# Optimization experiments

Measured on AMD Instinct MI355X. Metric: run time of the kernel, lower is better.

Reference implementation:

```python
import jax, jax.numpy as jnp
import numpy as np

TEMPERATURE = 0.07
SIM_THRESHOLD = 0.5


def setup_inputs() -> dict:
    key = jax.random.key(0)
    k1, k2 = jax.random.split(key)
    features = jax.random.normal(k1, (4096, 2, 128), dtype=jnp.float32)
    labels = jax.random.randint(k2, (4096, 100), 0, 2).astype(jnp.float32)
    return {"features": features, "labels": labels}


def reference(features, labels):
    B, V, D = features.shape

    # label Jaccard similarity -> positive/negative masks [B, B]
    intersection = labels @ labels.T
    row_sum = jnp.sum(labels, axis=1, keepdims=True)
    union = row_sum + row_sum.T - intersection
    similarity = intersection / (union + 1e-6)
    positive_mask = (similarity >= SIM_THRESHOLD).astype(jnp.float32)
    negative_mask = 1.0 - positive_mask

    # torch.cat(torch.unbind(features, dim=1), dim=0) -> [V*B, D] (view-major)
    contrast_feature = jnp.transpose(features, (1, 0, 2)).reshape(V * B, D)
    dot_similarities = (contrast_feature @ contrast_feature.T) / TEMPERATURE  # [VB, VB]

    # numerical stability: subtract detached row max over the FULL row
    logits_max = jax.lax.stop_gradient(jnp.max(dot_similarities, axis=1, keepdims=True))
    logits = dot_similarities - logits_max

    # only the top-left [B, B] block is ever indexed by the original loop
    e = jnp.exp(logits[:B, :B])
    pos_sum = jnp.sum(e * positive_mask, axis=1)  # [B]
    neg_sum = jnp.sum(e * negative_mask, axis=1)  # [B]

    has_pos = jnp.sum(positive_mask, axis=1) > 0  # rows with >=1 positive
    pos_safe = jnp.where(has_pos, pos_sum, 1.0)
    den_safe = jnp.where(has_pos, pos_sum + neg_sum, 1.0)
    per_row = -jnp.log(pos_safe / den_safe)

    count = jnp.sum(has_pos.astype(jnp.float32))
    loss = jnp.sum(jnp.where(has_pos, per_row, 0.0)) / jnp.maximum(count, 1.0)
    return loss
```

## Files before the change

### kernel.cpp

```cpp
#include <hip/hip_runtime.h>
#include <math.h>

#define B_ROWS 4096
#define DIM 128
#define LBL 100
#define NCHUNK 16
#define NTILE 32

typedef __attribute__((ext_vector_type(8))) short bf16x8;
typedef __attribute__((ext_vector_type(4))) float f32x4;

__device__ __forceinline__ unsigned f2bf(float x) {
  union { float f; unsigned u; } a; a.f = x;
  unsigned r = a.u + 0x7fffu + ((a.u >> 16) & 1u);
  return r >> 16;
}

__device__ __forceinline__ void lds_dma16(void* l, const void* g) {
  __builtin_amdgcn_global_load_lds(
      (const __attribute__((address_space(1))) void*)g,
      (__attribute__((address_space(3))) void*)l, 16, 0, 0);
}

__global__ void pack_kernel(const float* __restrict__ feat,
                            uint4* __restrict__ cf) {
  int g = blockIdx.x * 256 + threadIdx.x;
  int tile = g >> 11, o = g & 2047;
  int kc = o >> 7, q = o & 127;
  int r = q ^ kc;
  const float* src = feat + ((size_t)(tile * 128 + r)) * 256 + kc * 8;
  float4 a = *(const float4*)src;
  float4 b = *(const float4*)(src + 4);
  uint4 ov;
  ov.x = f2bf(a.x) | (f2bf(a.y) << 16);
  ov.y = f2bf(a.z) | (f2bf(a.w) << 16);
  ov.z = f2bf(b.x) | (f2bf(b.y) << 16);
  ov.w = f2bf(b.z) | (f2bf(b.w) << 16);
  cf[g] = ov;
}

__global__ void seedlabel_kernel(const float* __restrict__ feat,
                                 const float* __restrict__ labels,
                                 uint4* __restrict__ Lb,
                                 int* __restrict__ rsv,
                                 float* __restrict__ seedRaw) {
  int w = (int)((blockIdx.x * blockDim.x + threadIdx.x) >> 6);
  int lane = threadIdx.x & 63;
  const float2* src = (const float2*)(feat + (size_t)w * 256);
  float2 f = src[lane];
  float b0 = __uint_as_float(f2bf(f.x) << 16);
  float b1 = __uint_as_float(f2bf(f.y) << 16);
  float s = b0 * b0 + b1 * b1;
  #pragma unroll
  for (int off = 32; off >= 1; off >>= 1) s += __shfl_xor(s, off);
  float x0 = labels[(size_t)w * LBL + lane];
  float x1 = (lane < LBL - 64) ? labels[(size_t)w * LBL + 64 + lane] : 0.0f;
  unsigned long long m0 = __ballot(x0 != 0.0f);
  unsigned long long m1 = __ballot(x1 != 0.0f);
  if (lane == 0) {
    Lb[w] = make_uint4((unsigned)m0, (unsigned)(m0 >> 32),
                       (unsigned)m1, (unsigned)(m1 >> 32));
    rsv[w] = __popcll(m0) + __popcll(m1);
    seedRaw[w] = s - 0.15f;
  }
}

__launch_bounds__(256, 2)
__global__ void main_kernel(const uint4* __restrict__ cf,
                            const uint4* __restrict__ Lb,
                            const int* __restrict__ rsv,
                            const float* __restrict__ seedRaw,
                            float2* __restrict__ part) {
  __shared__ uint4 As[2048];
  __shared__ uint4 Bs[2048];
  const int tid = threadIdx.x;
  const int lane = tid & 63;
  const int l15 = lane & 15;
  const int quad = lane >> 4;
  const int wave = tid >> 6;
  const int wi = (wave & 1) * 64;
  const int wj = (wave >> 1) * 64;
  const int rowBase = blockIdx.x * 128;
  const float invT = 1.0f / 0.07f;

  #pragma unroll
  for (int it = 0; it < 8; ++it) {
    int flat = it * 256 + tid;
    lds_dma16(&As[flat], &cf[(size_t)blockIdx.x * 2048 + flat]);
  }

  float srow[16], p_s[16], n_s[16];
  #pragma unroll
  for (int ti = 0; ti < 4; ++ti)
    #pragma unroll
    for (int r = 0; r < 4; ++r) {
      srow[ti * 4 + r] = seedRaw[rowBase + wi + ti * 16 + quad * 4 + r];
      p_s[ti * 4 + r] = 0.f;
      n_s[ti * 4 + r] = 0.f;
    }

  const bf16x8* Asv = (const bf16x8*)As;
  const bf16x8* Bsv = (const bf16x8*)Bs;

  for (int jt = 0; jt < 2; ++jt) {
    const int colBase = blockIdx.y * 256 + jt * 128;
    __syncthreads();
    #pragma unroll
    for (int it = 0; it < 8; ++it) {
      int flat = it * 256 + tid;
      lds_dma16(&Bs[flat], &cf[(size_t)(colBase >> 7) * 2048 + flat]);
    }
    __syncthreads();

    uint4 clb[4];
    int crs[4];
    #pragma unroll
    for (int tj = 0; tj < 4; ++tj) {
      int gcol = colBase + wj + tj * 16 + l15;
      clb[tj] = Lb[gcol];
      crs[tj] = rsv[gcol];
    }

    f32x4 acc[4][4];
    #pragma unroll
    for (int ti = 0; ti < 4; ++ti)
      #pragma unroll
      for (int tj = 0; tj < 4; ++tj)
        acc[ti][tj] = (f32x4){0.f, 0.f, 0.f, 0.f};

    #pragma unroll
    for (int ks = 0; ks < 4; ++ks) {
      const int kc = ks * 4 + quad;
      const int abase = kc * 128 + wi + (l15 ^ kc);
      const int bbase = kc * 128 + wj + (l15 ^ kc);
      bf16x8 af[4], bfr[4];
      #pragma unroll
      for (int t = 0; t < 4; ++t) {
        af[t] = Asv[abase + t * 16];
        bfr[t] = Bsv[bbase + t * 16];
      }
      #pragma unroll
      for (int ti = 0; ti < 4; ++ti)
        #pragma unroll
        for (int tj = 0; tj < 4; ++tj)
          acc[ti][tj] = __builtin_amdgcn_mfma_f32_16x16x32_bf16(
              af[ti], bfr[tj], acc[ti][tj], 0, 0, 0);
    }

    #pragma unroll
    for (int ti = 0; ti < 4; ++ti)
      #pragma unroll
      for (int r = 0; r < 4; ++r) {
        int si = ti * 4 + r;
        float l0 = acc[ti][0][r], l1 = acc[ti][1][r];
        float l2 = acc[ti][2][r], l3 = acc[ti][3][r];
        float tm = fmaxf(fmaxf(l0, l1), fmaxf(l2, l3));
        if (tm > srow[si] - 6.3f) {
          int grow = rowBase + wi + ti * 16 + quad * 4 + r;
          uint4 la = Lb[grow];
          int ra = rsv[grow];
          float p = p_s[si], n = n_s[si];
          float lv[4] = {l0, l1, l2, l3};
          #pragma unroll
          for (int tj = 0; tj < 4; ++tj) {
            float e = __expf((lv[tj] - srow[si]) * invT);
            int inter = __popc(la.x & clb[tj].x) + __popc(la.y & clb[tj].y) +
                        __popc(la.z & clb[tj].z) + __popc(la.w & clb[tj].w);
            if (3 * inter > ra + crs[tj]) p += e; else n += e;
          }
          p_s[si] = p;
          n_s[si] = n;
        }
      }
  }

  #pragma unroll
  for (int si = 0; si < 16; ++si) {
    float p = p_s[si], n = n_s[si];
    #pragma unroll
    for (int off = 8; off >= 1; off >>= 1) {
      p += __shfl_xor(p, off);
      n += __shfl_xor(n, off);
    }
    p_s[si] = p;
    n_s[si] = n;
  }

  __syncthreads();
  float* mbuf = (float*)As;
  if (wj == 64 && l15 == 0) {
    #pragma unroll
    for (int ti = 0; ti < 4; ++ti)
      #pragma unroll
      for (int r = 0; r < 4; ++r) {
        int row = wi + ti * 16 + quad * 4 + r;
        int si = ti * 4 + r;
        mbuf[row * 2 + 0] = p_s[si];
        mbuf[row * 2 + 1] = n_s[si];
      }
  }
  __syncthreads();
  if (wj == 0 && l15 == 0) {
    #pragma unroll
    for (int ti = 0; ti < 4; ++ti)
      #pragma unroll
      for (int r = 0; r < 4; ++r) {
        int row = wi + ti * 16 + quad * 4 + r;
        int si = ti * 4 + r;
        float p = p_s[si] + mbuf[row * 2 + 0];
        float n = n_s[si] + mbuf[row * 2 + 1];
        part[(size_t)blockIdx.y * B_ROWS + rowBase + row] = make_float2(p, n);
      }
  }
}

__global__ void mergefin_kernel(const float2* __restrict__ part,
                                const int* __restrict__ rsv,
                                float* __restrict__ out) {
  __shared__ float red[8];
  int t = threadIdx.x;
  float per = 0.f, cnt = 0.f;
  #pragma unroll
  for (int i = 0; i < 16; ++i) {
    int row = i * 256 + t;
    float p = 0.f, n = 0.f;
    #pragma unroll
    for (int c = 0; c < NCHUNK; ++c) {
      float2 v = part[(size_t)c * B_ROWS + row];
      p += v.x;
      n += v.y;
    }
    if (rsv[row] > 0) {
      per += -logf(p / (p + n));
      cnt += 1.f;
    }
  }
  #pragma unroll
  for (int off = 32; off >= 1; off >>= 1) {
    per += __shfl_xor(per, off);
    cnt += __shfl_xor(cnt, off);
  }
  int wv = t >> 6;
  if ((t & 63) == 0) { red[wv * 2] = per; red[wv * 2 + 1] = cnt; }
  __syncthreads();
  if (t == 0) {
    float P = red[0] + red[2] + red[4] + red[6];
    float C = red[1] + red[3] + red[5] + red[7];
    out[0] = P / fmaxf(C, 1.0f);
  }
}

extern "C" void kernel_launch(void* const* d_in, const int* in_sizes, int n_in,
                              void* d_out, int out_size, void* d_ws, size_t ws_size,
                              hipStream_t stream) {
  const float* feat = (const float*)d_in[0];
  const float* labels = (const float*)d_in[1];
  float* out = (float*)d_out;
  char* ws = (char*)d_ws;
  uint4* cf = (uint4*)(ws + 0);
  uint4* Lbm = (uint4*)(ws + 1048576);
  int* rsv = (int*)(ws + 1114112);
  float* seedRaw = (float*)(ws + 1130496);
  float2* part = (float2*)(ws + 1146880);

  hipLaunchKernelGGL(pack_kernel, dim3(256), dim3(256), 0, stream, feat, cf);
  hipLaunchKernelGGL(seedlabel_kernel, dim3(1024), dim3(256), 0, stream,
                     feat, labels, Lbm, rsv, seedRaw);
  hipLaunchKernelGGL(main_kernel, dim3(NTILE, NCHUNK), dim3(256), 0, stream,
                     cf, Lbm, rsv, seedRaw, part);
  hipLaunchKernelGGL(mergefin_kernel, dim3(1), dim3(256), 0, stream,
                     part, rsv, out);
}
```

Before: 86.25 us.

## Use 32x32 one-tile-per-block grid, stage labels in LDS, parallelize merge with atomics

The main kernel now processes a single 128x128 tile per block on a 32x32 grid instead of two column tiles per block on a 32x16 grid. Both A and B tiles are loaded up front, and row and column label bitmasks, popcounts and seeds are staged once in shared memory. The pack kernel remaps thread indexing so global reads are coalesced per row and writes go to the swizzled layout. The single-block merge is replaced by a 16-block merge using atomics plus a tiny finish kernel. This adds more parallelism and removes serial tail work, at the cost of twice as many partial sums and an extra kernel launch.

Measured after the change: 85.01 us. About the same (-1.4%).

```diff
diff --git a/kernel.cpp b/kernel.cpp
--- a/kernel.cpp
+++ b/kernel.cpp
@@ -4,8 +4,7 @@
 #define B_ROWS 4096
 #define DIM 128
 #define LBL 100
-#define NCHUNK 16
-#define NTILE 32
+#define NCT 32
 
 typedef __attribute__((ext_vector_type(8))) short bf16x8;
 typedef __attribute__((ext_vector_type(4))) float f32x4;
@@ -23,11 +22,12 @@
 }
 
 __global__ void pack_kernel(const float* __restrict__ feat,
-                            uint4* __restrict__ cf) {
+                            uint4* __restrict__ cf,
+                            float* __restrict__ accum) {
+  if (blockIdx.x == 0 && threadIdx.x < 2) accum[threadIdx.x] = 0.0f;
   int g = blockIdx.x * 256 + threadIdx.x;
-  int tile = g >> 11, o = g & 2047;
-  int kc = o >> 7, q = o & 127;
-  int r = q ^ kc;
+  int tile = g >> 11, rem = g & 2047;
+  int r = rem >> 4, kc = rem & 15;
   const float* src = feat + ((size_t)(tile * 128 + r)) * 256 + kc * 8;
   float4 a = *(const float4*)src;
   float4 b = *(const float4*)(src + 4);
@@ -36,7 +36,7 @@
   ov.y = f2bf(a.z) | (f2bf(a.w) << 16);
   ov.z = f2bf(b.x) | (f2bf(b.y) << 16);
   ov.w = f2bf(b.z) | (f2bf(b.w) << 16);
-  cf[g] = ov;
+  cf[(size_t)tile * 2048 + kc * 128 + (r ^ kc)] = ov;
 }
 
 __global__ void seedlabel_kernel(const float* __restrict__ feat,
@@ -73,6 +73,11 @@
                             float2* __restrict__ part) {
   __shared__ uint4 As[2048];
   __shared__ uint4 Bs[2048];
+  __shared__ uint4 cLb[128];
+  __shared__ uint4 rLb[128];
+  __shared__ int   cRs[128];
+  __shared__ int   rRs[128];
+  __shared__ float sS[128];
   const int tid = threadIdx.x;
   const int lane = tid & 63;
   const int l15 = lane & 15;
@@ -81,98 +86,92 @@
   const int wi = (wave & 1) * 64;
   const int wj = (wave >> 1) * 64;
   const int rowBase = blockIdx.x * 128;
+  const int colBase = blockIdx.y * 128;
   const float invT = 1.0f / 0.07f;
 
   #pragma unroll
   for (int it = 0; it < 8; ++it) {
     int flat = it * 256 + tid;
     lds_dma16(&As[flat], &cf[(size_t)blockIdx.x * 2048 + flat]);
-  }
-
-  float srow[16], p_s[16], n_s[16];
+    lds_dma16(&Bs[flat], &cf[(size_t)blockIdx.y * 2048 + flat]);
+  }
+  if (tid < 128) {
+    cLb[tid] = Lb[colBase + tid];
+    cRs[tid] = rsv[colBase + tid];
+    sS[tid] = seedRaw[rowBase + tid];
+  } else {
+    int t = tid - 128;
+    rLb[t] = Lb[rowBase + t];
+    rRs[t] = rsv[rowBase + t];
+  }
+  __syncthreads();
+
+  float srow[16];
   #pragma unroll
   for (int ti = 0; ti < 4; ++ti)
     #pragma unroll
-    for (int r = 0; r < 4; ++r) {
-      srow[ti * 4 + r] = seedRaw[rowBase + wi + ti * 16 + quad * 4 + r];
-      p_s[ti * 4 + r] = 0.f;
-      n_s[ti * 4 + r] = 0.f;
-    }
+    for (int r = 0; r < 4; ++r)
+      srow[ti * 4 + r] = sS[wi + ti * 16 + quad * 4 + r];
 
   const bf16x8* Asv = (const bf16x8*)As;
   const bf16x8* Bsv = (const bf16x8*)Bs;
 
-  for (int jt = 0; jt < 2; ++jt) {
-    const int colBase = blockIdx.y * 256 + jt * 128;
-    __syncthreads();
-    #pragma unroll
-    for (int it = 0; it < 8; ++it) {
-      int flat = it * 256 + tid;
-      lds_dma16(&Bs[flat], &cf[(size_t)(colBase >> 7) * 2048 + flat]);
+  f32x4 acc[4][4];
+  #pragma unroll
+  for (int ti = 0; ti < 4; ++ti)
+    #pragma unroll
+    for (int tj = 0; tj < 4; ++tj)
+      acc[ti][tj] = (f32x4){0.f, 0.f, 0.f, 0.f};
+
+  #pragma unroll
+  for (int ks = 0; ks < 4; ++ks) {
+    const int kc = ks * 4 + quad;
+    const int abase = kc * 128 + wi + (l15 ^ kc);
+    const int bbase = kc * 128 + wj + (l15 ^ kc);
+    bf16x8 af[4], bfr[4];
+    #pragma unroll
+    for (int t = 0; t < 4; ++t) {
+      af[t] = Asv[abase + t * 16];
+      bfr[t] = Bsv[bbase + t * 16];
     }
-    __syncthreads();
-
-    uint4 clb[4];
-    int crs[4];
-    #pragma unroll
-    for (int tj = 0; tj < 4; ++tj) {
-      int gcol = colBase + wj + tj * 16 + l15;
-      clb[tj] = Lb[gcol];
-      crs[tj] = rsv[gcol];
-    }
-
-    f32x4 acc[4][4];
     #pragma unroll
     for (int ti = 0; ti < 4; ++ti)
       #pragma unroll
       for (int tj = 0; tj < 4; ++tj)
-        acc[ti][tj] = (f32x4){0.f, 0.f, 0.f, 0.f};
-
-    #pragma unroll
-    for (int ks = 0; ks < 4; ++ks) {
-      const int kc = ks * 4 + quad;
-      const int abase = kc * 128 + wi + (l15 ^ kc);
-      const int bbase = kc * 128 + wj + (l15 ^ kc);
-      bf16x8 af[4], bfr[4];
-      #pragma unroll
-      for (int t = 0; t < 4; ++t) {
-        af[t] = Asv[abase + t * 16];
-        bfr[t] = Bsv[bbase + t * 16];
+        acc[ti][tj] = __builtin_amdgcn_mfma_f32_16x16x32_bf16(
+            af[ti], bfr[tj], acc[ti][tj], 0, 0, 0);
+  }
+
+  float p_s[16], n_s[16];
+  #pragma unroll
+  for (int i = 0; i < 16; ++i) { p_s[i] = 0.f; n_s[i] = 0.f; }
+  #pragma unroll
+  for (int ti = 0; ti < 4; ++ti)
+    #pragma unroll
+    for (int r = 0; r < 4; ++r) {
+      int si = ti * 4 + r;
+      float l0 = acc[ti][0][r], l1 = acc[ti][1][r];
+      float l2 = acc[ti][2][r], l3 = acc[ti][3][r];
+      float tm = fmaxf(fmaxf(l0, l1), fmaxf(l2, l3));
+      if (tm > srow[si] - 6.3f) {
+        int lrow = wi + ti * 16 + quad * 4 + r;
+        uint4 la = rLb[lrow];
+        int ra = rRs[lrow];
+        float p = 0.f, n = 0.f;
+        float lv[4] = {l0, l1, l2, l3};
+        #pragma unroll
+        for (int tj = 0; tj < 4; ++tj) {
+          float e = __expf((lv[tj] - srow[si]) * invT);
+          int lcol = wj + tj * 16 + l15;
+          uint4 lb = cLb[lcol];
+          int inter = __popc(la.x & lb.x) + __popc(la.y & lb.y) +
+                      __popc(la.z & lb.z) + __popc(la.w & lb.w);
+          if (3 * inter > ra + cRs[lcol]) p += e; else n += e;
+        }
+        p_s[si] = p;
+        n_s[si] = n;
       }
-      #pragma unroll
-      for (int ti = 0; ti < 4; ++ti)
-        #pragma unroll
-        for (int tj = 0; tj < 4; ++tj)
-          acc[ti][tj] = __builtin_amdgcn_mfma_f32_16x16x32_bf16(
-              af[ti], bfr[tj], acc[ti][tj], 0, 0, 0);
     }
-
-    #pragma unroll
-    for (int ti = 0; ti < 4; ++ti)
-      #pragma unroll
-      for (int r = 0; r < 4; ++r) {
-        int si = ti * 4 + r;
-        float l0 = acc[ti][0][r], l1 = acc[ti][1][r];
-        float l2 = acc[ti][2][r], l3 = acc[ti][3][r];
-        float tm = fmaxf(fmaxf(l0, l1), fmaxf(l2, l3));
-        if (tm > srow[si] - 6.3f) {
-          int grow = rowBase + wi + ti * 16 + quad * 4 + r;
-          uint4 la = Lb[grow];
-          int ra = rsv[grow];
-          float p = p_s[si], n = n_s[si];
-          float lv[4] = {l0, l1, l2, l3};
-          #pragma unroll
-          for (int tj = 0; tj < 4; ++tj) {
-            float e = __expf((lv[tj] - srow[si]) * invT);
-            int inter = __popc(la.x & clb[tj].x) + __popc(la.y & clb[tj].y) +
-                        __popc(la.z & clb[tj].z) + __popc(la.w & clb[tj].w);
-            if (3 * inter > ra + crs[tj]) p += e; else n += e;
-          }
-          p_s[si] = p;
-          n_s[si] = n;
-        }
-      }
-  }
 
   #pragma unroll
   for (int si = 0; si < 16; ++si) {
@@ -214,40 +213,36 @@
   }
 }
 
-__global__ void mergefin_kernel(const float2* __restrict__ part,
-                                const int* __restrict__ rsv,
-                                float* __restrict__ out) {
-  __shared__ float red[8];
-  int t = threadIdx.x;
+__global__ void merge_kernel(const float2* __restrict__ part,
+                             const int* __restrict__ rsv,
+                             float* __restrict__ accum) {
+  int row = blockIdx.x * 256 + threadIdx.x;
+  float p = 0.f, n = 0.f;
+  #pragma unroll
+  for (int c = 0; c < NCT; ++c) {
+    float2 v = part[(size_t)c * B_ROWS + row];
+    p += v.x;
+    n += v.y;
+  }
   float per = 0.f, cnt = 0.f;
-  #pragma unroll
-  for (int i = 0; i < 16; ++i) {
-    int row = i * 256 + t;
-    float p = 0.f, n = 0.f;
-    #pragma unroll
-    for (int c = 0; c < NCHUNK; ++c) {
-      float2 v = part[(size_t)c * B_ROWS + row];
-      p += v.x;
-      n += v.y;
-    }
-    if (rsv[row] > 0) {
-      per += -logf(p / (p + n));
-      cnt += 1.f;
-    }
+  if (rsv[row] > 0) {
+    per = -logf(p / (p + n));
+    cnt = 1.f;
   }
   #pragma unroll
   for (int off = 32; off >= 1; off >>= 1) {
     per += __shfl_xor(per, off);
     cnt += __shfl_xor(cnt, off);
   }
-  int wv = t >> 6;
-  if ((t & 63) == 0) { red[wv * 2] = per; red[wv * 2 + 1] = cnt; }
-  __syncthreads();
-  if (t == 0) {
-    float P = red[0] + red[2] + red[4] + red[6];
-    float C = red[1] + red[3] + red[5] + red[7];
-    out[0] = P / fmaxf(C, 1.0f);
-  }
+  if ((threadIdx.x & 63) == 0) {
+    atomicAdd(accum + 0, per);
+    atomicAdd(accum + 1, cnt);
+  }
+}
+
+__global__ void fin_kernel(const float* __restrict__ accum,
+                           float* __restrict__ out) {
+  out[0] = accum[0] / fmaxf(accum[1], 1.0f);
 }
 
 extern "C" void kernel_launch(void* const* d_in, const int* in_sizes, int n_in,
@@ -262,12 +257,15 @@
   int* rsv = (int*)(ws + 1114112);
   float* seedRaw = (float*)(ws + 1130496);
   float2* part = (float2*)(ws + 1146880);
-
-  hipLaunchKernelGGL(pack_kernel, dim3(256), dim3(256), 0, stream, feat, cf);
+  float* accum = (float*)(ws + 1146880 + 1048576);
+
+  hipLaunchKernelGGL(pack_kernel, dim3(256), dim3(256), 0, stream,
+                     feat, cf, accum);
   hipLaunchKernelGGL(seedlabel_kernel, dim3(1024), dim3(256), 0, stream,
                      feat, labels, Lbm, rsv, seedRaw);
-  hipLaunchKernelGGL(main_kernel, dim3(NTILE, NCHUNK), dim3(256), 0, stream,
+  hipLaunchKernelGGL(main_kernel, dim3(NCT, NCT), dim3(256), 0, stream,
                      cf, Lbm, rsv, seedRaw, part);
-  hipLaunchKernelGGL(mergefin_kernel, dim3(1), dim3(256), 0, stream,
-                     part, rsv, out);
-}
+  hipLaunchKernelGGL(merge_kernel, dim3(B_ROWS / 256), dim3(256), 0, stream,
+                     part, rsv, accum);
+  hipLaunchKernelGGL(fin_kernel, dim3(1), dim3(1), 0, stream, accum, out);
+}
```
